# Optimization experiments

Measured on AMD Instinct MI355X. Metric: run time of the kernel, lower is better.

Reference implementation:

```python
import jax, jax.numpy as jnp
import numpy as np
import math

B, S, D, H = 4, 2048, 512, 8
HD = D // H

def setup_inputs() -> dict:
    key = jax.random.key(0)
    ks = jax.random.split(key, 12)
    s_hd = 1.0 / math.sqrt(HD)
    s_d = 1.0 / math.sqrt(D)
    return {
        "q": jax.random.normal(ks[0], (B, S, D), jnp.float32),
        "k": jax.random.normal(ks[1], (B, S, D), jnp.float32),
        "v": jax.random.normal(ks[2], (B, S, D), jnp.float32),
        # torch nn.Linear(head_dim, head_dim): weight [HD, HD], bias [HD]
        "Wq": jax.random.uniform(ks[3], (HD, HD), jnp.float32, -s_hd, s_hd),
        "bq": jax.random.uniform(ks[4], (HD,), jnp.float32, -s_hd, s_hd),
        "Wk": jax.random.uniform(ks[5], (HD, HD), jnp.float32, -s_hd, s_hd),
        "bk": jax.random.uniform(ks[6], (HD,), jnp.float32, -s_hd, s_hd),
        "Wv": jax.random.uniform(ks[7], (HD, HD), jnp.float32, -s_hd, s_hd),
        "bv": jax.random.uniform(ks[8], (HD,), jnp.float32, -s_hd, s_hd),
        # output projection nn.Linear(d, d)
        "Wo": jax.random.uniform(ks[9], (D, D), jnp.float32, -s_d, s_d),
        "bo": jax.random.uniform(ks[10], (D,), jnp.float32, -s_d, s_d),
        # LayerNorm(d) affine params
        "gamma": jnp.ones((D,), jnp.float32),
        "beta": jnp.zeros((D,), jnp.float32),
    }

def _layernorm(x, gamma, beta, eps=1e-5):
    mu = jnp.mean(x, axis=-1, keepdims=True)
    var = jnp.var(x, axis=-1, keepdims=True)
    return (x - mu) * jax.lax.rsqrt(var + eps) * gamma + beta

def reference(q, k, v, Wq, bq, Wk, bk, Wv, bv, Wo, bo, gamma, beta):
    batch, q_len = q.shape[0], q.shape[1]
    # split heads: [B, L, H, HD]; per-head Linear shares one weight across heads
    Qh = q.reshape(batch, q_len, H, HD) @ Wq.T + bq
    Kh = k.reshape(batch, k.shape[1], H, HD) @ Wk.T + bk
    Vh = v.reshape(batch, v.shape[1], H, HD) @ Wv.T + bv
    # scores scaled by sqrt(d) (faithful to source, NOT sqrt(head_dim))
    scores = jnp.einsum('bqhd,bkhd->bhqk', Qh, Kh) / math.sqrt(D)
    attn = jax.nn.softmax(scores, axis=-1)
    out = jnp.einsum('bhqk,bkhd->bqhd', attn, Vh)
    concat = out.reshape(batch, q_len, D)
    lin = concat @ Wo.T + bo
    # AddNorm quirk: residual added AFTER LayerNorm (dropout = identity in eval)
    return q + _layernorm(lin, gamma, beta)
```

## Files before the change

### kernel.cpp

```cpp
#include <hip/hip_runtime.h>
#include <hip/hip_bf16.h>
#include <math.h>
#include <stdint.h>

#define B 4
#define S 2048
#define D 512
#define H 8
#define HD 64

typedef __attribute__((ext_vector_type(4))) int   int4v;
typedef __attribute__((ext_vector_type(8))) short short8;
typedef __attribute__((ext_vector_type(4))) short short4v;
typedef __attribute__((ext_vector_type(4))) float f32x4;

__device__ __forceinline__ unsigned short bfr(float x) {
    __bf16 h = (__bf16)x;
    union { __bf16 b; unsigned short s; } u; u.b = h; return u.s;
}
__device__ __forceinline__ float b2f(unsigned short s) {
    union { unsigned u; float f; } v; v.u = (unsigned)s << 16; return v.f;
}
__device__ __forceinline__ float ex2(float x) {
#if __has_builtin(__builtin_amdgcn_exp2f)
    return __builtin_amdgcn_exp2f(x);
#else
    return exp2f(x);
#endif
}
__device__ __forceinline__ short8 cvt8(const float* p) {
    float4 f0 = *(const float4*)p;
    float4 f1 = *(const float4*)(p + 4);
    short8 s8;
    s8[0] = (short)bfr(f0.x); s8[1] = (short)bfr(f0.y);
    s8[2] = (short)bfr(f0.z); s8[3] = (short)bfr(f0.w);
    s8[4] = (short)bfr(f1.x); s8[5] = (short)bfr(f1.y);
    s8[6] = (short)bfr(f1.z); s8[7] = (short)bfr(f1.w);
    return s8;
}

#define QSCALE 0.06377229601488305f
#define MFIX 4.0f

typedef const __attribute__((address_space(1))) unsigned char g8_t;
typedef __attribute__((address_space(3))) unsigned char l8_t;
__device__ __forceinline__ void gl_lds16(const unsigned short* g, unsigned short* l) {
#if __has_builtin(__builtin_amdgcn_global_load_lds)
    __builtin_amdgcn_global_load_lds((g8_t*)g, (l8_t*)l, 16, 0, 0);
#else
    int lane = threadIdx.x & 63;
    ((int4v*)l)[lane] = *(const int4v*)g;
#endif
}

__global__ __launch_bounds__(256) void qkv_mfma_kernel(
    const float* __restrict__ q, const float* __restrict__ k,
    const float* __restrict__ v,
    const float* __restrict__ Wq, const float* __restrict__ bq,
    const float* __restrict__ Wk, const float* __restrict__ bk,
    const float* __restrict__ Wv, const float* __restrict__ bv,
    const float* __restrict__ Wo, unsigned short* __restrict__ WoB,
    unsigned short* __restrict__ Qh, unsigned short* __restrict__ Kh,
    unsigned short* __restrict__ VtG)
{
    const int t = threadIdx.x;
    const int bid = blockIdx.x;
    if (bid >= 1536) {
        int i = (bid - 1536) * 1024 + t * 4;
        float4 f = *(const float4*)(Wo + i);
        short4v s;
        s[0] = (short)bfr(f.x); s[1] = (short)bfr(f.y);
        s[2] = (short)bfr(f.z); s[3] = (short)bfr(f.w);
        *(short4v*)(WoB + i) = s;
        return;
    }

    __shared__ __align__(16) unsigned short Wl[64 * 72];
    __shared__ __align__(16) unsigned short Tb[4][1536];

    const int x   = bid / 512;
    const int r_  = bid - x * 512;
    const int bh  = r_ >> 4;
    const int stg = r_ & 15;
    const int b = bh >> 3, h = bh & 7;
    const int L = t & 63, w = t >> 6;
    const int c = L & 15, qd = L >> 4;

    const float* Wf     = (x == 0) ? Wq : (x == 1) ? Wk : Wv;
    const float* bias_p = (x == 0) ? bq : (x == 1) ? bk : bv;
    const float* X      = (x == 0) ? q  : (x == 1) ? k  : v;

    unsigned short* Tw = Tb[w];

    {
        int row = t >> 2, col = (t & 3) * 16;
        *(short8*)&Wl[row * 72 + col]     = cvt8(Wf + t * 16);
        *(short8*)&Wl[row * 72 + col + 8] = cvt8(Wf + t * 16 + 8);
    }
    __syncthreads();

    short8 wf[4][2];
    #pragma unroll
    for (int nt = 0; nt < 4; ++nt)
        #pragma unroll
        for (int kc = 0; kc < 2; ++kc)
            wf[nt][kc] = *(const short8*)&Wl[(16 * nt + c) * 72 + kc * 32 + 8 * qd];

    if (x < 2) {
        float bias[4];
        #pragma unroll
        for (int nt = 0; nt < 4; ++nt) bias[nt] = bias_p[16 * nt + c];
        const float sc = (x == 0) ? QSCALE : 1.0f;
        #pragma unroll
        for (int ti = 0; ti < 2; ++ti) {
            const int st = stg * 8 + w * 2 + ti;
            const float* xrow = X + ((size_t)(b * S + st * 16 + c)) * D + h * HD;
            short8 af0 = cvt8(xrow + 8 * qd);
            short8 af1 = cvt8(xrow + 32 + 8 * qd);
            f32x4 acc[4];
            #pragma unroll
            for (int nt = 0; nt < 4; ++nt) {
                acc[nt] = (f32x4){bias[nt], bias[nt], bias[nt], bias[nt]};
                acc[nt] = __builtin_amdgcn_mfma_f32_16x16x32_bf16(af0, wf[nt][0], acc[nt], 0, 0, 0);
                acc[nt] = __builtin_amdgcn_mfma_f32_16x16x32_bf16(af1, wf[nt][1], acc[nt], 0, 0, 0);
            }
            #pragma unroll
            for (int nt = 0; nt < 4; ++nt)
                #pragma unroll
                for (int r = 0; r < 4; ++r)
                    Tw[(4 * qd + r) * 72 + 16 * nt + c] = bfr(acc[nt][r] * sc);
            int rw = L >> 2, cg_ = (L & 3) * 16;
            short8 s0 = *(const short8*)&Tw[rw * 72 + cg_];
            short8 s1 = *(const short8*)&Tw[rw * 72 + cg_ + 8];
            unsigned short* O = ((x == 0) ? Qh : Kh)
                              + ((size_t)(b * H + h) * S + st * 16) * HD;
            *(short8*)&O[rw * HD + cg_]     = s0;
            *(short8*)&O[rw * HD + cg_ + 8] = s1;
        }
    } else {
        f32x4 bias4[4];
        #pragma unroll
        for (int nt = 0; nt < 4; ++nt) {
            float4 bb4 = *(const float4*)(bias_p + 16 * nt + 4 * qd);
            bias4[nt] = (f32x4){bb4.x, bb4.y, bb4.z, bb4.w};
        }
        #pragma unroll
        for (int ti = 0; ti < 2; ++ti) {
            const int st = stg * 8 + w * 2 + ti;
            const float* xrow = X + ((size_t)(b * S + st * 16 + c)) * D + h * HD;
            short8 af0 = cvt8(xrow + 8 * qd);
            short8 af1 = cvt8(xrow + 32 + 8 * qd);
            f32x4 acc[4];
            #pragma unroll
            for (int nt = 0; nt < 4; ++nt) {
                acc[nt] = bias4[nt];
                acc[nt] = __builtin_amdgcn_mfma_f32_16x16x32_bf16(wf[nt][0], af0, acc[nt], 0, 0, 0);
                acc[nt] = __builtin_amdgcn_mfma_f32_16x16x32_bf16(wf[nt][1], af1, acc[nt], 0, 0, 0);
            }
            #pragma unroll
            for (int nt = 0; nt < 4; ++nt)
                #pragma unroll
                for (int r = 0; r < 4; ++r)
                    Tw[(16 * nt + 4 * qd + r) * 24 + c] = bfr(acc[nt][r]);
            short8 s0 = *(const short8*)&Tw[L * 24];
            short8 s1 = *(const short8*)&Tw[L * 24 + 8];
            unsigned short* O = VtG + (size_t)(b * H + h) * HD * S;
            *(short8*)&O[(size_t)L * S + st * 16]     = s0;
            *(short8*)&O[(size_t)L * S + st * 16 + 8] = s1;
        }
    }
}

__global__ __launch_bounds__(256, 4) void attn_kernel(
    const unsigned short* __restrict__ Qh, const unsigned short* __restrict__ Kh,
    const unsigned short* __restrict__ VtG, unsigned short* __restrict__ accPb,
    float* __restrict__ lP)
{
    __shared__ __align__(16) unsigned short Ks[2][4096];
    __shared__ __align__(16) unsigned short Vs[2][4096];

    const int idx = blockIdx.x;
    const int bh = idx & 31;
    const int rem = idx >> 5;
    const int qt = rem >> 1;
    const int ks = rem & 1;
    const int b = bh >> 3, h = bh & 7;
    const int t = threadIdx.x;
    const int w = t >> 6, L = t & 63;
    const int c = L & 15, qd = L >> 4;

    const unsigned short* Kb = Kh + ((size_t)bh * S + ks * 1024) * HD;
    const unsigned short* Vb = VtG + (size_t)bh * HD * S + ks * 1024;

    short8 qf[2][2];
    #pragma unroll
    for (int qg = 0; qg < 2; ++qg)
        #pragma unroll
        for (int kc = 0; kc < 2; ++kc)
            qf[qg][kc] = *(const short8*)(Qh
                + ((size_t)bh * S + qt * 128 + w * 32 + qg * 16 + c) * HD
                + kc * 32 + 8 * qd);

    f32x4 acc[2][4];
    float lrun[2] = {0.f, 0.f};
    #pragma unroll
    for (int qg = 0; qg < 2; ++qg)
        #pragma unroll
        for (int dt = 0; dt < 4; ++dt) acc[qg][dt] = (f32x4){0.f, 0.f, 0.f, 0.f};

    const int sd = t >> 3, sj = t & 7;
    const int sp = sj >> 2, smt = (sj >> 1) & 1;
    const int sqa = (2 * sj) & 3, sqb = (2 * sj + 1) & 3;
    int voff0 = (((0 * 2 + sp) * 64 + sqa * 16 + 0) * 8 + smt * 4) * 2;
    int voff1 = (((0 * 2 + sp) * 64 + sqb * 16 + 0) * 8 + smt * 4) * 2;

    int4v vpre[2];
    #pragma unroll
    for (int i = 0; i < 2; ++i) {
        int bi = w + 4 * i;
        gl_lds16(Kb + (size_t)(16 * (bi >> 1) + c) * HD + (bi & 1) * 32 + qd * 8,
                 &Ks[0][bi * 512]);
        vpre[i] = *(const int4v*)(Vb + (size_t)(sd + 32 * i) * S + 8 * sj);
    }

    for (int it = 0; it < 16; ++it) {
        const int cur = it & 1, nxt = cur ^ 1;
        unsigned char* VsB = (unsigned char*)&Vs[cur][0];
        #pragma unroll
        for (int i = 0; i < 2; ++i) {
            int d = sd + 32 * i;
            int dt = d >> 4, cc = d & 15;
            union { int4v v; short4v h[2]; } u; u.v = vpre[i];
            int o0 = voff0 + dt * 2048 + cc * 16;
            int o1 = voff1 + dt * 2048 + cc * 16;
            o0 ^= ((o0 >> 8) & 3) << 5;
            o1 ^= ((o1 >> 8) & 3) << 5;
            *(short4v*)(VsB + o0) = u.h[0];
            *(short4v*)(VsB + o1) = u.h[1];
        }
        __syncthreads();
        if (it + 1 < 16) {
            int n1 = (it + 1) * 64;
            #pragma unroll
            for (int i = 0; i < 2; ++i) {
                int bi = w + 4 * i;
                gl_lds16(Kb + (size_t)(n1 + 16 * (bi >> 1) + c) * HD + (bi & 1) * 32 + qd * 8,
                         &Ks[nxt][bi * 512]);
                vpre[i] = *(const int4v*)(Vb + (size_t)(sd + 32 * i) * S + n1 + 8 * sj);
            }
        }

        const unsigned short* KsC = Ks[cur];
        const unsigned char* VsR = (const unsigned char*)&Vs[cur][0];

        short4v pa[2][4];
        #pragma unroll
        for (int mt = 0; mt < 4; ++mt) {
            short8 a0 = *(const short8*)(KsC + (mt * 2 + 0) * 512 + L * 8);
            short8 a1 = *(const short8*)(KsC + (mt * 2 + 1) * 512 + L * 8);
            #pragma unroll
            for (int qg = 0; qg < 2; ++qg) {
                f32x4 stv = (f32x4){-MFIX, -MFIX, -MFIX, -MFIX};
                __builtin_amdgcn_s_setprio(1);
                stv = __builtin_amdgcn_mfma_f32_16x16x32_bf16(a0, qf[qg][0], stv, 0, 0, 0);
                stv = __builtin_amdgcn_mfma_f32_16x16x32_bf16(a1, qf[qg][1], stv, 0, 0, 0);
                __builtin_amdgcn_s_setprio(0);
                float p0 = ex2(stv[0]), p1 = ex2(stv[1]);
                float p2 = ex2(stv[2]), p3 = ex2(stv[3]);
                lrun[qg] += (p0 + p1) + (p2 + p3);
                short4v p_;
                p_[0] = (short)bfr(p0); p_[1] = (short)bfr(p1);
                p_[2] = (short)bfr(p2); p_[3] = (short)bfr(p3);
                pa[qg][mt] = p_;
            }
        }

        #pragma unroll
        for (int dt = 0; dt < 4; ++dt)
            #pragma unroll
            for (int p = 0; p < 2; ++p) {
                int roff = ((dt * 2 + p) * 512 + L * 8) * 2;
                roff ^= ((roff >> 8) & 3) << 5;
                union { short8 v8; short4v h[2]; } u;
                u.v8 = *(const short8*)(VsR + roff);
#if __has_builtin(__builtin_amdgcn_mfma_f32_16x16x16bf16_1k)
                __builtin_amdgcn_s_setprio(1);
                #pragma unroll
                for (int qg = 0; qg < 2; ++qg) {
                    acc[qg][dt] = __builtin_amdgcn_mfma_f32_16x16x16bf16_1k(
                        pa[qg][2 * p + 0], u.h[0], acc[qg][dt], 0, 0, 0);
                    acc[qg][dt] = __builtin_amdgcn_mfma_f32_16x16x16bf16_1k(
                        pa[qg][2 * p + 1], u.h[1], acc[qg][dt], 0, 0, 0);
                }
                __builtin_amdgcn_s_setprio(0);
#else
                __builtin_amdgcn_s_setprio(1);
                #pragma unroll
                for (int qg = 0; qg < 2; ++qg) {
                    short8 pz0 = {pa[qg][2 * p + 0][0], pa[qg][2 * p + 0][1],
                                  pa[qg][2 * p + 0][2], pa[qg][2 * p + 0][3], 0, 0, 0, 0};
                    short8 pz1 = {pa[qg][2 * p + 1][0], pa[qg][2 * p + 1][1],
                                  pa[qg][2 * p + 1][2], pa[qg][2 * p + 1][3], 0, 0, 0, 0};
                    short8 v0 = {u.h[0][0], u.h[0][1], u.h[0][2], u.h[0][3], 0, 0, 0, 0};
                    short8 v1 = {u.h[1][0], u.h[1][1], u.h[1][2], u.h[1][3], 0, 0, 0, 0};
                    acc[qg][dt] = __builtin_amdgcn_mfma_f32_16x16x32_bf16(pz0, v0, acc[qg][dt], 0, 0, 0);
                    acc[qg][dt] = __builtin_amdgcn_mfma_f32_16x16x32_bf16(pz1, v1, acc[qg][dt], 0, 0, 0);
                }
                __builtin_amdgcn_s_setprio(0);
#endif
            }
    }

    const int q0 = qt * 128 + w * 32;
    unsigned short* accPp = accPb + (size_t)ks * ((size_t)B * S * D)
                          + ((size_t)b * S + q0) * D + h * HD;
    #pragma unroll
    for (int qg = 0; qg < 2; ++qg) {
        float lr = lrun[qg];
        lr += __shfl_xor(lr, 16);
        lr += __shfl_xor(lr, 32);
        if (qd == 0)
            lP[(size_t)ks * ((size_t)B * H * S) + (size_t)bh * S + q0 + qg * 16 + c] = lr;
        #pragma unroll
        for (int dt = 0; dt < 4; ++dt)
            #pragma unroll
            for (int r = 0; r < 4; ++r)
                accPp[(size_t)(qg * 16 + 4 * qd + r) * D + 16 * dt + c]
                    = bfr(acc[qg][dt][r]);
    }
}

__global__ __launch_bounds__(1024) void oproj_ln_kernel(
    const unsigned short* __restrict__ accPb, const float* __restrict__ lP,
    const unsigned short* __restrict__ WoB,
    const float* __restrict__ bo, const float* __restrict__ gamma,
    const float* __restrict__ beta, const float* __restrict__ qin,
    float* __restrict__ out)
{
    __shared__ __align__(16) unsigned short As[32 * 520];
    __shared__ float red[2][32][17];
    __shared__ float linv_s[32][8];
    __shared__ float mu_s2[32], rs_s2[32];

    const int t = threadIdx.x;
    const int r0 = blockIdx.x * 32;
    const int w = t >> 6, L = t & 63;
    const int c = L & 15, qd = L >> 4;
    const int n0 = w * 32;
    const size_t NEh = (size_t)B * S * D;
    const size_t BHS = (size_t)B * H * S;

    if (t < 256) {
        int row = t >> 3, hh = t & 7;
        int bb = r0 >> 11;
        int ss = (r0 & (S - 1)) + row;
        float l0 = lP[(size_t)(bb * H + hh) * S + ss];
        float l1 = lP[BHS + (size_t)(bb * H + hh) * S + ss];
        linv_s[row][hh] = 1.f / (l0 + l1);
    }
    __syncthreads();

    #pragma unroll
    for (int i = 0; i < 4; ++i) {
        int flat = t + 1024 * i;
        int row = flat >> 7, cg4 = flat & 127;
        int col = cg4 * 4;
        size_t gi = (size_t)(r0 + row) * D + col;
        short4v a0 = *(const short4v*)(accPb + gi);
        short4v a1 = *(const short4v*)(accPb + NEh + gi);
        float li = linv_s[row][col >> 6];
        short4v s;
        #pragma unroll
        for (int j = 0; j < 4; ++j)
            s[j] = (short)bfr((b2f((unsigned short)a0[j])
                             + b2f((unsigned short)a1[j])) * li);
        *(short4v*)&As[row * 520 + col] = s;
    }
    __syncthreads();

    f32x4 acc[2][2];
    #pragma unroll
    for (int nt = 0; nt < 2; ++nt) {
        float bv_ = bo[n0 + 16 * nt + c];
        acc[0][nt] = (f32x4){bv_, bv_, bv_, bv_};
        acc[1][nt] = (f32x4){bv_, bv_, bv_, bv_};
    }

    for (int kc = 0; kc < 16; ++kc) {
        short8 a0 = *(const short8*)&As[c * 520 + kc * 32 + 8 * qd];
        short8 a1 = *(const short8*)&As[(16 + c) * 520 + kc * 32 + 8 * qd];
        #pragma unroll
        for (int nt = 0; nt < 2; ++nt) {
            short8 bf = *(const short8*)(WoB + (size_t)(n0 + 16 * nt + c) * D
                                         + kc * 32 + 8 * qd);
            acc[0][nt] = __builtin_amdgcn_mfma_f32_16x16x32_bf16(a0, bf, acc[0][nt], 0, 0, 0);
            acc[1][nt] = __builtin_amdgcn_mfma_f32_16x16x32_bf16(a1, bf, acc[1][nt], 0, 0, 0);
        }
    }

    float sm[2][4], sq[2][4];
    #pragma unroll
    for (int mt = 0; mt < 2; ++mt)
        #pragma unroll
        for (int r = 0; r < 4; ++r) { sm[mt][r] = 0.f; sq[mt][r] = 0.f; }
    #pragma unroll
    for (int mt = 0; mt < 2; ++mt)
        #pragma unroll
        for (int nt = 0; nt < 2; ++nt)
            #pragma unroll
            for (int r = 0; r < 4; ++r) {
                float x_ = acc[mt][nt][r];
                sm[mt][r] += x_; sq[mt][r] += x_ * x_;
            }
    #pragma unroll
    for (int mask = 1; mask <= 8; mask <<= 1)
        #pragma unroll
        for (int mt = 0; mt < 2; ++mt)
            #pragma unroll
            for (int r = 0; r < 4; ++r) {
                sm[mt][r] += __shfl_xor(sm[mt][r], mask);
                sq[mt][r] += __shfl_xor(sq[mt][r], mask);
            }
    if (c == 0) {
        #pragma unroll
        for (int mt = 0; mt < 2; ++mt)
            #pragma unroll
            for (int r = 0; r < 4; ++r) {
                red[0][mt * 16 + 4 * qd + r][w] = sm[mt][r];
                red[1][mt * 16 + 4 * qd + r][w] = sq[mt][r];
            }
    }
    __syncthreads();

    if (t < 32) {
        float s_ = 0.f, q_ = 0.f;
        #pragma unroll
        for (int w_ = 0; w_ < 16; ++w_) { s_ += red[0][t][w_]; q_ += red[1][t][w_]; }
        float mu_ = s_ * (1.f / D);
        float var = q_ * (1.f / D) - mu_ * mu_;
        mu_s2[t] = mu_;
        rs_s2[t] = rsqrtf(var + 1e-5f);
    }
    __syncthreads();

    #pragma unroll
    for (int nt = 0; nt < 2; ++nt) {
        int n = n0 + 16 * nt + c;
        float g = gamma[n], be = beta[n];
        #pragma unroll
        for (int mt = 0; mt < 2; ++mt)
            #pragma unroll
            for (int r = 0; r < 4; ++r) {
                int m = mt * 16 + 4 * qd + r;
                size_t gi = (size_t)(r0 + m) * D + n;
                out[gi] = qin[gi] + (acc[mt][nt][r] - mu_s2[m]) * rs_s2[m] * g + be;
            }
    }
}

extern "C" void kernel_launch(void* const* d_in, const int* in_sizes, int n_in,
                              void* d_out, int out_size, void* d_ws, size_t ws_size,
                              hipStream_t stream) {
    const float* q     = (const float*)d_in[0];
    const float* k     = (const float*)d_in[1];
    const float* v     = (const float*)d_in[2];
    const float* Wq    = (const float*)d_in[3];
    const float* bq    = (const float*)d_in[4];
    const float* Wk    = (const float*)d_in[5];
    const float* bk    = (const float*)d_in[6];
    const float* Wv    = (const float*)d_in[7];
    const float* bv    = (const float*)d_in[8];
    const float* Wo    = (const float*)d_in[9];
    const float* bo    = (const float*)d_in[10];
    const float* gamma = (const float*)d_in[11];
    const float* beta  = (const float*)d_in[12];
    float* out = (float*)d_out;

    const size_t NE = (size_t)B * S * D;
    unsigned short* wsu = (unsigned short*)d_ws;
    unsigned short* Qh    = wsu;
    unsigned short* Kh    = wsu + NE;
    unsigned short* VtG   = wsu + 2 * NE;
    unsigned short* WoB   = wsu + 3 * NE;
    unsigned short* accPb = WoB + (size_t)D * D;
    float* lP = (float*)(accPb + 2 * NE);

    hipLaunchKernelGGL(qkv_mfma_kernel, dim3(1536 + 256), dim3(256), 0, stream,
                       q, k, v, Wq, bq, Wk, bk, Wv, bv, Wo, WoB, Qh, Kh, VtG);
    hipLaunchKernelGGL(attn_kernel, dim3(1024), dim3(256), 0, stream,
                       Qh, Kh, VtG, accPb, lP);
    hipLaunchKernelGGL(oproj_ln_kernel, dim3(B * S / 32), dim3(1024), 0, stream,
                       accPb, lP, WoB, bo, gamma, beta, q, out);
}
```

Before: 192.7 us.

## Use K=32 MFMA for PV and compute softmax row sums via MFMA with ones

```diff
diff --git a/kernel.cpp b/kernel.cpp
--- a/kernel.cpp
+++ b/kernel.cpp
@@ -202,17 +202,21 @@
                 + kc * 32 + 8 * qd);
 
     f32x4 acc[2][4];
-    float lrun[2] = {0.f, 0.f};
-    #pragma unroll
-    for (int qg = 0; qg < 2; ++qg)
+    f32x4 lacc[2];
+    #pragma unroll
+    for (int qg = 0; qg < 2; ++qg) {
+        lacc[qg] = (f32x4){0.f, 0.f, 0.f, 0.f};
         #pragma unroll
         for (int dt = 0; dt < 4; ++dt) acc[qg][dt] = (f32x4){0.f, 0.f, 0.f, 0.f};
+    }
+
+    const short8 ones8 = {0x3F80, 0x3F80, 0x3F80, 0x3F80,
+                          0x3F80, 0x3F80, 0x3F80, 0x3F80};
 
     const int sd = t >> 3, sj = t & 7;
-    const int sp = sj >> 2, smt = (sj >> 1) & 1;
-    const int sqa = (2 * sj) & 3, sqb = (2 * sj + 1) & 3;
-    int voff0 = (((0 * 2 + sp) * 64 + sqa * 16 + 0) * 8 + smt * 4) * 2;
-    int voff1 = (((0 * 2 + sp) * 64 + sqb * 16 + 0) * 8 + smt * 4) * 2;
+    const int s3 = sj & 3;
+    const int vslotp = sj >> 2;
+    const int vadd = (s3 & 1) * 256 + (s3 >> 1) * 4;
 
     int4v vpre[2];
     #pragma unroll
@@ -225,18 +229,13 @@
 
     for (int it = 0; it < 16; ++it) {
         const int cur = it & 1, nxt = cur ^ 1;
-        unsigned char* VsB = (unsigned char*)&Vs[cur][0];
         #pragma unroll
         for (int i = 0; i < 2; ++i) {
             int d = sd + 32 * i;
-            int dt = d >> 4, cc = d & 15;
+            int os = ((d >> 4) * 2 + vslotp) * 512 + (d & 15) * 8 + vadd;
             union { int4v v; short4v h[2]; } u; u.v = vpre[i];
-            int o0 = voff0 + dt * 2048 + cc * 16;
-            int o1 = voff1 + dt * 2048 + cc * 16;
-            o0 ^= ((o0 >> 8) & 3) << 5;
-            o1 ^= ((o1 >> 8) & 3) << 5;
-            *(short4v*)(VsB + o0) = u.h[0];
-            *(short4v*)(VsB + o1) = u.h[1];
+            *(short4v*)&Vs[cur][os]       = u.h[0];
+            *(short4v*)&Vs[cur][os + 128] = u.h[1];
         }
         __syncthreads();
         if (it + 1 < 16) {
@@ -251,9 +250,9 @@
         }
 
         const unsigned short* KsC = Ks[cur];
-        const unsigned char* VsR = (const unsigned char*)&Vs[cur][0];
-
-        short4v pa[2][4];
+        const unsigned short* VsC = Vs[cur];
+
+        short8 ps[2][2];
         #pragma unroll
         for (int mt = 0; mt < 4; ++mt) {
             short8 a0 = *(const short8*)(KsC + (mt * 2 + 0) * 512 + L * 8);
@@ -267,48 +266,29 @@
                 __builtin_amdgcn_s_setprio(0);
                 float p0 = ex2(stv[0]), p1 = ex2(stv[1]);
                 float p2 = ex2(stv[2]), p3 = ex2(stv[3]);
-                lrun[qg] += (p0 + p1) + (p2 + p3);
-                short4v p_;
-                p_[0] = (short)bfr(p0); p_[1] = (short)bfr(p1);
-                p_[2] = (short)bfr(p2); p_[3] = (short)bfr(p3);
-                pa[qg][mt] = p_;
-            }
-        }
-
+                const int pp = mt >> 1, hl = (mt & 1) * 4;
+                ps[qg][pp][hl + 0] = (short)bfr(p0);
+                ps[qg][pp][hl + 1] = (short)bfr(p1);
+                ps[qg][pp][hl + 2] = (short)bfr(p2);
+                ps[qg][pp][hl + 3] = (short)bfr(p3);
+            }
+        }
+
+        __builtin_amdgcn_s_setprio(1);
+        #pragma unroll
+        for (int pp = 0; pp < 2; ++pp) {
+            lacc[0] = __builtin_amdgcn_mfma_f32_16x16x32_bf16(ps[0][pp], ones8, lacc[0], 0, 0, 0);
+            lacc[1] = __builtin_amdgcn_mfma_f32_16x16x32_bf16(ps[1][pp], ones8, lacc[1], 0, 0, 0);
+        }
         #pragma unroll
         for (int dt = 0; dt < 4; ++dt)
             #pragma unroll
-            for (int p = 0; p < 2; ++p) {
-                int roff = ((dt * 2 + p) * 512 + L * 8) * 2;
-                roff ^= ((roff >> 8) & 3) << 5;
-                union { short8 v8; short4v h[2]; } u;
-                u.v8 = *(const short8*)(VsR + roff);
-#if __has_builtin(__builtin_amdgcn_mfma_f32_16x16x16bf16_1k)
-                __builtin_amdgcn_s_setprio(1);
-                #pragma unroll
-                for (int qg = 0; qg < 2; ++qg) {
-                    acc[qg][dt] = __builtin_amdgcn_mfma_f32_16x16x16bf16_1k(
-                        pa[qg][2 * p + 0], u.h[0], acc[qg][dt], 0, 0, 0);
-                    acc[qg][dt] = __builtin_amdgcn_mfma_f32_16x16x16bf16_1k(
-                        pa[qg][2 * p + 1], u.h[1], acc[qg][dt], 0, 0, 0);
-                }
-                __builtin_amdgcn_s_setprio(0);
-#else
-                __builtin_amdgcn_s_setprio(1);
-                #pragma unroll
-                for (int qg = 0; qg < 2; ++qg) {
-                    short8 pz0 = {pa[qg][2 * p + 0][0], pa[qg][2 * p + 0][1],
-                                  pa[qg][2 * p + 0][2], pa[qg][2 * p + 0][3], 0, 0, 0, 0};
-                    short8 pz1 = {pa[qg][2 * p + 1][0], pa[qg][2 * p + 1][1],
-                                  pa[qg][2 * p + 1][2], pa[qg][2 * p + 1][3], 0, 0, 0, 0};
-                    short8 v0 = {u.h[0][0], u.h[0][1], u.h[0][2], u.h[0][3], 0, 0, 0, 0};
-                    short8 v1 = {u.h[1][0], u.h[1][1], u.h[1][2], u.h[1][3], 0, 0, 0, 0};
-                    acc[qg][dt] = __builtin_amdgcn_mfma_f32_16x16x32_bf16(pz0, v0, acc[qg][dt], 0, 0, 0);
-                    acc[qg][dt] = __builtin_amdgcn_mfma_f32_16x16x32_bf16(pz1, v1, acc[qg][dt], 0, 0, 0);
-                }
-                __builtin_amdgcn_s_setprio(0);
-#endif
-            }
+            for (int pp = 0; pp < 2; ++pp) {
+                short8 vb = *(const short8*)(VsC + (dt * 2 + pp) * 512 + L * 8);
+                acc[0][dt] = __builtin_amdgcn_mfma_f32_16x16x32_bf16(ps[0][pp], vb, acc[0][dt], 0, 0, 0);
+                acc[1][dt] = __builtin_amdgcn_mfma_f32_16x16x32_bf16(ps[1][pp], vb, acc[1][dt], 0, 0, 0);
+            }
+        __builtin_amdgcn_s_setprio(0);
     }
 
     const int q0 = qt * 128 + w * 32;
@@ -316,11 +296,12 @@
                           + ((size_t)b * S + q0) * D + h * HD;
     #pragma unroll
     for (int qg = 0; qg < 2; ++qg) {
-        float lr = lrun[qg];
-        lr += __shfl_xor(lr, 16);
-        lr += __shfl_xor(lr, 32);
-        if (qd == 0)
-            lP[(size_t)ks * ((size_t)B * H * S) + (size_t)bh * S + q0 + qg * 16 + c] = lr;
+        if (c == 0) {
+            #pragma unroll
+            for (int r = 0; r < 4; ++r)
+                lP[(size_t)ks * ((size_t)B * H * S) + (size_t)bh * S
+                   + q0 + qg * 16 + 4 * qd + r] = lacc[qg][r];
+        }
         #pragma unroll
         for (int dt = 0; dt < 4; ++dt)
             #pragma unroll
```

Result: faster. 180.7 us, median of 2 (-6.2%).
